# Performance work log

Measured on AMD Instinct MI355X. Metric: run time of the kernel, lower is better.

Reference implementation:

```python
import jax, jax.numpy as jnp
import numpy as np

B, N, K = 8, 2048, 20
NC = 50
EPS = 1e-5
SLOPE = 0.2


def _knn(xt, k):
    # xt: [B, N, C]; negative squared euclidean distance, top-k (includes self)
    xx = jnp.sum(xt * xt, axis=-1)                      # [B, N]
    inner = jnp.einsum('bnc,bmc->bnm', xt, xt)          # [B, N, N]
    dist = 2.0 * inner - xx[:, :, None] - xx[:, None, :]
    return jax.lax.top_k(dist, k)[1]                    # [B, N, k] int32


def _edge_conv(xt, w, g, b, k):
    # xt: [B, N, C]; w: [O, 2C]; BatchNorm2d over (B, N, k) per out-channel.
    idx = _knn(xt, k)
    nbr = xt[jnp.arange(B)[:, None, None], idx]          # [B, N, k, C]
    ctr = jnp.broadcast_to(xt[:, :, None, :], nbr.shape)
    edge = jnp.concatenate([nbr - ctr, ctr], axis=-1)    # [B, N, k, 2C]
    h = jnp.einsum('bnkc,oc->bnko', edge, w)             # 1x1 conv, no bias
    mu = jnp.mean(h, axis=(0, 1, 2))
    var = jnp.var(h, axis=(0, 1, 2))
    h = (h - mu) / jnp.sqrt(var + EPS) * g + b
    h = jnp.where(h > 0, h, SLOPE * h)                   # LeakyReLU(0.2)
    return jnp.max(h, axis=2)                            # max over k -> [B, N, O]


def _bn1d(y, g, b):
    mu = jnp.mean(y, axis=0)
    var = jnp.var(y, axis=0)
    return (y - mu) / jnp.sqrt(var + EPS) * g + b


def setup_inputs() -> dict:
    key = jax.random.key(0)
    ks = jax.random.split(key, 20)

    def rn(k, shape, scale):
        return jax.random.normal(k, shape, dtype=jnp.float32) * scale

    d = {
        'x': rn(ks[0], (B * N, 3), 1.0),
        'pos': rn(ks[1], (B * N, 3), 1.0),
        'batch': jnp.repeat(jnp.arange(B, dtype=jnp.int64), N),
        'edge_index': jax.random.randint(ks[2], (2, B * N), 0, B * N, dtype=jnp.int64),
        # EdgeConv 1x1 conv weights [out, in], BN gamma/beta
        'w1': rn(ks[3], (64, 6), 0.3),   'g1': jnp.ones(64),  'b1': jnp.zeros(64),
        'w2': rn(ks[4], (64, 128), 0.1), 'g2': jnp.ones(64),  'b2': jnp.zeros(64),
        'w3': rn(ks[5], (128, 128), 0.1),'g3': jnp.ones(128), 'b3': jnp.zeros(128),
        'w4': rn(ks[6], (256, 256), 0.08),'g4': jnp.ones(256),'b4': jnp.zeros(256),
        # lin1: Linear(512,1024)+ReLU+BN1d(1024)
        'lw1': rn(ks[7], (512, 1024), 0.04), 'lb1': jnp.zeros(1024),
        'lg1': jnp.ones(1024), 'lbb1': jnp.zeros(1024),
        # mlp: [1024->256 +ReLU+BN] -> [256->128 +ReLU+BN] -> Lin(128, NC)
        'mw1': rn(ks[8], (1024, 256), 0.03), 'mb1': jnp.zeros(256),
        'mg1': jnp.ones(256), 'mbb1': jnp.zeros(256),
        'mw2': rn(ks[9], (256, 128), 0.06), 'mb2': jnp.zeros(128),
        'mg2': jnp.ones(128), 'mbb2': jnp.zeros(128),
        'hw': rn(ks[10], (128, NC), 0.09), 'hb': jnp.zeros(NC),
    }
    return d


def reference(x, pos, batch, edge_index,
              w1, g1, b1, w2, g2, b2, w3, g3, b3, w4, g4, b4,
              lw1, lb1, lg1, lbb1,
              mw1, mb1, mg1, mbb1, mw2, mb2, mg2, mbb2,
              hw, hb):
    # batch is sorted with N points per cloud -> static reshape
    xt = x.reshape(B, N, 3)
    x1 = _edge_conv(xt, w1, g1, b1, K)   # [B, N, 64]
    x2 = _edge_conv(x1, w2, g2, b2, K)   # [B, N, 64]
    x3 = _edge_conv(x2, w3, g3, b3, K)   # [B, N, 128]
    x4 = _edge_conv(x3, w4, g4, b4, K)   # [B, N, 256]
    cat = jnp.concatenate([x1, x2, x3, x4], axis=-1)  # [B, N, 512]
    h = cat.reshape(B * N, 512)
    h = _bn1d(jax.nn.relu(h @ lw1 + lb1), lg1, lbb1)
    h = _bn1d(jax.nn.relu(h @ mw1 + mb1), mg1, mbb1)   # dropout = identity (eval)
    h = _bn1d(jax.nn.relu(h @ mw2 + mb2), mg2, mbb2)
    logits = h @ hw + hb
    return jax.nn.log_softmax(logits, axis=1)
```

## Files before the change

### kernel.cpp

```cpp
#include <hip/hip_runtime.h>
#include <math.h>

#define NB 8
#define NP 2048
#define KNBR 20
#define NROWS (NB*NP)
#define SLOPEV 0.2f
#define EPSV 1e-5f

typedef short s8v __attribute__((ext_vector_type(8)));
typedef float f4v __attribute__((ext_vector_type(4)));

__device__ __forceinline__ unsigned short f2bf(float f) {
    union { float f; unsigned u; } v; v.f = f;
    unsigned r = v.u + 0x7FFFu + ((v.u >> 16) & 1u);
    return (unsigned short)(r >> 16);
}

#define DK 16
__global__ __launch_bounds__(256, 2) void gemm64_dist(
    const double* __restrict__ A, int lda, int Kd,
    const double* __restrict__ xx, double* __restrict__ Cm, int batch0)
{
    __shared__ double As[DK][130];
    __shared__ double Bs[DK][66];
    const int tid = threadIdx.x;
    const int tx = tid & 15, ty = tid >> 4;
    const int bb = blockIdx.y;
    const int x  = blockIdx.x;
    int bi = (int)((sqrtf(4.0f * x + 1.0f) - 1.0f) * 0.5f);
    while (bi * (bi + 1) > x) --bi;
    while ((bi + 1) * (bi + 2) <= x) ++bi;
    const int bj = x - bi * (bi + 1);
    const int row0 = bi * 128, col0 = bj * 64;
    const double* Ab  = A + (size_t)(batch0 + bb) * NP * lda;
    double*       Cb  = Cm + (size_t)bb * NP * NP;
    const double* xxb = xx + (size_t)(batch0 + bb) * NP;

    double acc[8][4];
#pragma unroll
    for (int i = 0; i < 8; ++i)
#pragma unroll
        for (int j = 0; j < 4; ++j) acc[i][j] = 0.0;

    const int ma = tid >> 1, ka = (tid & 1) * 8;
    const int mb = tid >> 2, kb = (tid & 3) * 4;

    for (int kc = 0; kc < Kd; kc += DK) {
        const double* ap = Ab + (size_t)(row0 + ma) * lda + kc + ka;
#pragma unroll
        for (int i = 0; i < 8; ++i) {
            const int k2 = kc + ka + i;
            As[ka + i][ma] = (k2 < Kd) ? ap[i] : 0.0;
        }
        const double* bp = Ab + (size_t)(col0 + mb) * lda + kc + kb;
#pragma unroll
        for (int i = 0; i < 4; ++i) {
            const int k2 = kc + kb + i;
            Bs[kb + i][mb] = (k2 < Kd) ? bp[i] : 0.0;
        }
        __syncthreads();
#pragma unroll
        for (int k = 0; k < DK; ++k) {
            double a[8], b[4];
            *(double2*)&a[0] = *(const double2*)&As[k][ty * 4];
            *(double2*)&a[2] = *(const double2*)&As[k][ty * 4 + 2];
            *(double2*)&a[4] = *(const double2*)&As[k][64 + ty * 4];
            *(double2*)&a[6] = *(const double2*)&As[k][64 + ty * 4 + 2];
            *(double2*)&b[0] = *(const double2*)&Bs[k][tx * 4];
            *(double2*)&b[2] = *(const double2*)&Bs[k][tx * 4 + 2];
#pragma unroll
            for (int i = 0; i < 8; ++i)
#pragma unroll
                for (int j = 0; j < 4; ++j) acc[i][j] = fma(a[i], b[j], acc[i][j]);
        }
        __syncthreads();
    }

#pragma unroll
    for (int i = 0; i < 8; ++i) {
        const int r = row0 + ty * 4 + (i & 3) + ((i >> 2) << 6);
        const double xr = xxb[r];
#pragma unroll
        for (int j = 0; j < 4; ++j) {
            const int c = col0 + tx * 4 + j;
            const double a2 = 2.0 * acc[i][j];
            const double xc = xxb[c];
            Cb[(size_t)r * NP + c] = (a2 - xr) - xc;
            Cb[(size_t)c * NP + r] = (a2 - xc) - xr;
        }
    }
}

__global__ __launch_bounds__(256, 2) void gemm64(
    const double* __restrict__ A, int lda,
    const double* __restrict__ Bm, int ldb,
    double* __restrict__ P, double* __restrict__ Q, int O, int Kd)
{
    __shared__ double As[DK][130];
    __shared__ double Bs[DK][66];
    const int tid = threadIdx.x;
    const int tx = tid & 15, ty = tid >> 4;
    const int lin = blockIdx.y * gridDim.x + blockIdx.x;
    const int bx = lin / gridDim.y;
    const int by = lin - bx * gridDim.y;
    const int row0 = by * 128, col0 = bx * 64;

    double acc[8][4];
#pragma unroll
    for (int i = 0; i < 8; ++i)
#pragma unroll
        for (int j = 0; j < 4; ++j) acc[i][j] = 0.0;

    const int ma = tid >> 1, ka = (tid & 1) * 8;
    const int mb = tid >> 2, kb = (tid & 3) * 4;

    for (int kc = 0; kc < Kd; kc += DK) {
        const double* ap = A + (size_t)(row0 + ma) * lda + kc + ka;
#pragma unroll
        for (int i = 0; i < 8; ++i) {
            const int k2 = kc + ka + i;
            As[ka + i][ma] = (k2 < Kd) ? ap[i] : 0.0;
        }
        const double* bp = Bm + (size_t)(col0 + mb) * ldb + kc + kb;
#pragma unroll
        for (int i = 0; i < 4; ++i) {
            const int k2 = kc + kb + i;
            Bs[kb + i][mb] = (k2 < Kd) ? bp[i] : 0.0;
        }
        __syncthreads();
#pragma unroll
        for (int k = 0; k < DK; ++k) {
            double a[8], b[4];
            *(double2*)&a[0] = *(const double2*)&As[k][ty * 4];
            *(double2*)&a[2] = *(const double2*)&As[k][ty * 4 + 2];
            *(double2*)&a[4] = *(const double2*)&As[k][64 + ty * 4];
            *(double2*)&a[6] = *(const double2*)&As[k][64 + ty * 4 + 2];
            *(double2*)&b[0] = *(const double2*)&Bs[k][tx * 4];
            *(double2*)&b[2] = *(const double2*)&Bs[k][tx * 4 + 2];
#pragma unroll
            for (int i = 0; i < 8; ++i)
#pragma unroll
                for (int j = 0; j < 4; ++j) acc[i][j] = fma(a[i], b[j], acc[i][j]);
        }
        __syncthreads();
    }

    double* dst = (col0 < O) ? P : Q;
    const int cbase = (col0 < O) ? col0 : (col0 - O);
#pragma unroll
    for (int i = 0; i < 8; ++i) {
        const int r = row0 + ty * 4 + (i & 3) + ((i >> 2) << 6);
#pragma unroll
        for (int j = 0; j < 4; ++j) {
            const int c = cbase + tx * 4 + j;
            dst[(size_t)r * O + c] = acc[i][j];
        }
    }
}

__global__ __launch_bounds__(256) void gemm_bf16(
    const float* __restrict__ A, int lda,
    const unsigned short* __restrict__ W,
    float* __restrict__ C, int ldc,
    int Kd,
    const float* __restrict__ bias,
    const float* __restrict__ a_ss)
{
    __shared__ unsigned short As[4][64][8];
    __shared__ unsigned short Bs[4][128][8];
    const int tid = threadIdx.x;
    const int wave = tid >> 6, lane = tid & 63;
    const int quad = lane >> 4, l15 = lane & 15;
    const int row0 = blockIdx.y * 64, col0 = blockIdx.x * 128;

    f4v acc[4][2];
#pragma unroll
    for (int mt = 0; mt < 4; ++mt)
#pragma unroll
        for (int nt = 0; nt < 2; ++nt) acc[mt][nt] = (f4v){0.f, 0.f, 0.f, 0.f};

    const int ar = tid >> 2, akc = tid & 3;
    const int br = tid >> 1, bkc = (tid & 1) * 2;

    for (int kc0 = 0; kc0 < Kd; kc0 += 32) {
        {
            const float* ap = A + (size_t)(row0 + ar) * lda + kc0 + akc * 8;
            float t0[8];
            *(float4*)&t0[0] = *(const float4*)ap;
            *(float4*)&t0[4] = *(const float4*)(ap + 4);
            if (a_ss) {
                const int kb = kc0 + akc * 8;
#pragma unroll
                for (int i = 0; i < 8; ++i)
                    t0[i] = fmaf(t0[i], a_ss[kb + i], a_ss[Kd + kb + i]);
            }
            unsigned short u[8];
#pragma unroll
            for (int i = 0; i < 8; ++i) u[i] = f2bf(t0[i]);
            *(uint4*)&As[akc][ar][0] = *(const uint4*)&u[0];
        }
        {
            const unsigned short* wp = W + (size_t)(col0 + br) * Kd + kc0 + bkc * 8;
            uint4 q0 = *(const uint4*)wp;
            uint4 q1 = *(const uint4*)(wp + 8);
            *(uint4*)&Bs[bkc][br][0]     = q0;
            *(uint4*)&Bs[bkc + 1][br][0] = q1;
        }
        __syncthreads();

        s8v a[4], b[2];
#pragma unroll
        for (int mt = 0; mt < 4; ++mt)
            a[mt] = *(const s8v*)&As[quad][mt * 16 + l15][0];
#pragma unroll
        for (int nt = 0; nt < 2; ++nt)
            b[nt] = *(const s8v*)&Bs[quad][wave * 32 + nt * 16 + l15][0];
#pragma unroll
        for (int mt = 0; mt < 4; ++mt)
#pragma unroll
            for (int nt = 0; nt < 2; ++nt)
                acc[mt][nt] = __builtin_amdgcn_mfma_f32_16x16x32_bf16(
                    a[mt], b[nt], acc[mt][nt], 0, 0, 0);
        __syncthreads();
    }

#pragma unroll
    for (int mt = 0; mt < 4; ++mt)
#pragma unroll
        for (int nt = 0; nt < 2; ++nt) {
            const int col = col0 + wave * 32 + nt * 16 + l15;
            const float bi = bias[col];
#pragma unroll
            for (int r = 0; r < 4; ++r) {
                const int row = row0 + mt * 16 + quad * 4 + r;
                float v = acc[mt][nt][r] + bi;
                v = fmaxf(v, 0.f);
                C[(size_t)row * ldc + col] = v;
            }
        }
}

#define GBK 16
__global__ __launch_bounds__(256, 2) void gemm_f32(
    const float* __restrict__ A, int lda,
    const float* __restrict__ Bm, int ldb,
    float* __restrict__ Cm, int ldc,
    int M, int Nn, int Kd, int mode,
    const float* __restrict__ bias,
    const float* __restrict__ a_ss)
{
    __shared__ float As[GBK][132];
    __shared__ float Bs[GBK][132];
    const int tid = threadIdx.x;
    const int tx = tid & 15, ty = tid >> 4;
    const int lin = blockIdx.y * gridDim.x + blockIdx.x;
    const int bx = lin / gridDim.y;
    const int by = lin - bx * gridDim.y;
    const int row0 = by * 128, col0 = bx * 128;
    float acc[8][8];
#pragma unroll
    for (int i = 0; i < 8; ++i)
#pragma unroll
        for (int j = 0; j < 8; ++j) acc[i][j] = 0.f;

    const int m  = tid >> 1;
    const int kk = (tid & 1) * 8;

    for (int kc = 0; kc < Kd; kc += GBK) {
        const int gc = col0 + m;
        const float* ap = A  + (size_t)(row0 + m) * lda + kc + kk;
        const float* bp = Bm + (size_t)gc * ldb + kc + kk;
#pragma unroll
        for (int i = 0; i < 8; ++i) {
            const int k2 = kc + kk + i;
            float v = 0.f;
            if (k2 < Kd) {
                v = ap[i];
                if (a_ss) v = fmaf(v, a_ss[k2], a_ss[Kd + k2]);
            }
            As[kk + i][m] = v;
        }
#pragma unroll
        for (int i = 0; i < 8; ++i) {
            const int k2 = kc + kk + i;
            float v = 0.f;
            if (gc < Nn && k2 < Kd) v = bp[i];
            Bs[kk + i][m] = v;
        }
        __syncthreads();
#pragma unroll
        for (int k = 0; k < GBK; ++k) {
            float4 a0 = *(const float4*)&As[k][ty * 4];
            float4 a1 = *(const float4*)&As[k][64 + ty * 4];
            float4 b0 = *(const float4*)&Bs[k][tx * 4];
            float4 b1 = *(const float4*)&Bs[k][64 + tx * 4];
            float a[8] = {a0.x, a0.y, a0.z, a0.w, a1.x, a1.y, a1.z, a1.w};
            float b[8] = {b0.x, b0.y, b0.z, b0.w, b1.x, b1.y, b1.z, b1.w};
#pragma unroll
            for (int i = 0; i < 8; ++i)
#pragma unroll
                for (int j = 0; j < 8; ++j) acc[i][j] = fmaf(a[i], b[j], acc[i][j]);
        }
        __syncthreads();
    }

#pragma unroll
    for (int i = 0; i < 8; ++i) {
        const int row = row0 + ty * 4 + (i & 3) + ((i >> 2) << 6);
        if (row >= M) continue;
#pragma unroll
        for (int h = 0; h < 2; ++h) {
            const int c0 = col0 + tx * 4 + (h << 6);
#pragma unroll
            for (int j = 0; j < 4; ++j) {
                const int col = c0 + j;
                if (col < Nn) {
                    float t = acc[i][h * 4 + j];
                    if (mode == 2)      t = fmaxf(t + bias[col], 0.f);
                    else if (mode == 3) t = t + bias[col];
                    Cm[(size_t)row * ldc + col] = t;
                }
            }
        }
    }
}

__global__ void f2d_kernel(const float* __restrict__ in, double* __restrict__ out, long n)
{
    long t = (long)blockIdx.x * 256 + threadIdx.x;
    if (t < n) out[t] = (double)in[t];
}
__global__ void d2f_kernel(const double* __restrict__ in, float* __restrict__ out, long n)
{
    long t = (long)blockIdx.x * 256 + threadIdx.x;
    if (t < n) out[t] = (float)in[t];
}

__global__ void xx_kernel_d(const double* __restrict__ F, int lda, int C,
                            double* __restrict__ xx)
{
    int r = blockIdx.x * 256 + threadIdx.x;
    if (r >= NROWS) return;
    const double* p = F + (long)r * lda;
    double s = 0.0;
    for (int c = 0; c < C; ++c) { double v = p[c]; s = fma(v, v, s); }
    xx[r] = s;
}

__global__ void wmod_kernel_d(const float* __restrict__ w, double* __restrict__ wm,
                              int O, int C)
{
    int t = blockIdx.x * 256 + threadIdx.x;
    if (t >= O * C) return;
    int o = t / C, c = t - o * C;
    double a = (double)w[o * 2 * C + c];
    double b = (double)w[o * 2 * C + C + c];
    wm[o * C + c] = a;
    wm[(O + o) * C + c] = b - a;
}

__global__ void transpose_kernel(const float* __restrict__ in, float* __restrict__ out,
                                 int R, int C)
{
    long t = (long)blockIdx.x * 256 + threadIdx.x;
    if (t >= (long)R * C) return;
    int r = (int)(t / C), c = (int)(t - (long)r * C);
    out[(long)c * R + r] = in[t];
}

__global__ void transpose_bf(const float* __restrict__ in, unsigned short* __restrict__ out,
                             int R, int C)
{
    long t = (long)blockIdx.x * 256 + threadIdx.x;
    if (t >= (long)R * C) return;
    int r = (int)(t / C), c = (int)(t - (long)r * C);
    out[(long)c * R + r] = f2bf(in[t]);
}

__global__ __launch_bounds__(256) void topk2(const double* __restrict__ D,
                                             int* __restrict__ out, int batch0)
{
    const int lane = threadIdx.x & 63;
    const int bb   = blockIdx.y;
    const int row  = blockIdx.x * 4 + (threadIdx.x >> 6);
    const double* rp = D + (size_t)bb * NP * NP + (size_t)row * NP;
    double v[32];
#pragma unroll
    for (int j = 0; j < 16; ++j) {
        double2 p = *(const double2*)&rp[j * 128 + lane * 2];
        v[2 * j] = p.x; v[2 * j + 1] = p.y;
    }
    double lbest = v[0];
    int    lidx  = lane * 2;
#pragma unroll
    for (int q = 1; q < 32; ++q) {
        const int col = ((q >> 1) << 7) + lane * 2 + (q & 1);
        if (v[q] > lbest) { lbest = v[q]; lidx = col; }
    }

    int* op = out + ((size_t)(batch0 + bb) * NP + row) * KNBR;
    const int jbase = (batch0 + bb) * NP;

    for (int it = 0; it < KNBR; ++it) {
        double best = lbest; int bidx = lidx;
#pragma unroll
        for (int off = 32; off >= 1; off >>= 1) {
            double ov = __shfl_xor(best, off, 64);
            int    oi = __shfl_xor(bidx, off, 64);
            if (ov > best || (ov == best && oi < bidx)) { best = ov; bidx = oi; }
        }
        if (lane == 0) op[it] = jbase + bidx;
        if (lane == ((bidx >> 1) & 63)) {
            const int q = (((bidx >> 7) << 1) | (bidx & 1));
#pragma unroll
            for (int qq = 0; qq < 32; ++qq) if (qq == q) v[qq] = -INFINITY;
            lbest = v[0]; lidx = lane * 2;
#pragma unroll
            for (int qq = 1; qq < 32; ++qq) {
                const int col = ((qq >> 1) << 7) + lane * 2 + (qq & 1);
                if (v[qq] > lbest) { lbest = v[qq]; lidx = col; }
            }
        }
    }
}

__global__ __launch_bounds__(256) void edge_gather(const double* __restrict__ P,
                                                   const double* __restrict__ Q,
                                                   const int* __restrict__ idx,
                                                   int O, int shiftO,
                                                   double* __restrict__ sums,
                                                   double* __restrict__ catOut, int ldo)
{
    const int tid = threadIdx.x;
    const int o = tid & (O - 1);
    const int q = tid >> shiftO;
    const int nsub = 256 >> shiftO;
    const int lin = blockIdx.x;
    const int r0 = (lin & 7) * NP + (lin >> 3) * 16;
    double s = 0.0, ss = 0.0;
    for (int r = r0 + q; r < r0 + 16; r += nsub) {
        const double qv = Q[(size_t)r * O + o];
        const int* ip = idx + r * KNBR;
        double m = -INFINITY;
        for (int k = 0; k < KNBR; ++k) {
            const int j = ip[k];
            const double v = P[(size_t)j * O + o] + qv;
            s += v; ss = fma(v, v, ss);
            m = fmax(m, v);
        }
        catOut[(size_t)r * ldo + o] = m;
    }
    __shared__ double red[256];
    red[tid] = s; __syncthreads();
    if (q == 0) for (int qq = 1; qq < nsub; ++qq) s += red[o + (qq << shiftO)];
    __syncthreads();
    red[tid] = ss; __syncthreads();
    if (q == 0) {
        for (int qq = 1; qq < nsub; ++qq) ss += red[o + (qq << shiftO)];
        atomicAdd(&sums[o], s);
        atomicAdd(&sums[O + o], ss);
    }
}

__global__ void bn_finalize_d(const double* __restrict__ sums,
                              const float* __restrict__ g, const float* __restrict__ b,
                              double* __restrict__ ss, int O, double invCnt)
{
    int o = blockIdx.x * 256 + threadIdx.x;
    if (o >= O) return;
    double mu  = sums[o] * invCnt;
    double var = sums[O + o] * invCnt - mu * mu;
    double is  = 1.0 / sqrt(var + 1e-5);
    double sc  = (double)g[o] * is;
    ss[o] = sc;
    ss[O + o] = (double)b[o] - mu * sc;
}

__global__ __launch_bounds__(256) void bn_apply(double* __restrict__ catOut, int ldo,
                                                const double* __restrict__ ssb,
                                                int O, int shiftO,
                                                const double* __restrict__ P,
                                                const double* __restrict__ Q,
                                                const int* __restrict__ idx)
{
    const int t = blockIdx.x * 256 + threadIdx.x;
    const int o = t & (O - 1);
    const int r = t >> shiftO;
    const double sc = ssb[o], sh = ssb[O + o];
    double v = catOut[(size_t)r * ldo + o];
    if (sc < 0.0) {
        const double qv = Q[(size_t)r * O + o];
        const int* ip = idx + r * KNBR;
        double m = INFINITY;
        for (int k = 0; k < KNBR; ++k)
            m = fmin(m, P[(size_t)ip[k] * O + o] + qv);
        v = m;
    }
    double u = fma(v, sc, sh);
    u = u > 0.0 ? u : 0.2 * u;
    catOut[(size_t)r * ldo + o] = u;
}

__global__ void col_stats(const float* __restrict__ Y, int ncol,
                          float* __restrict__ sums)
{
    int c  = blockIdx.x * 128 + threadIdx.x;
    int r0 = blockIdx.y * 256;
    float s = 0.f, ss = 0.f;
    for (int r = r0; r < r0 + 256; ++r) {
        float v = Y[(long)r * ncol + c];
        s += v; ss = fmaf(v, v, ss);
    }
    atomicAdd(&sums[c], s);
    atomicAdd(&sums[ncol + c], ss);
}

__global__ void bn_finalize_f(const float* __restrict__ sums,
                              const float* __restrict__ g, const float* __restrict__ b,
                              float* __restrict__ ss, int O, float invCnt)
{
    int o = blockIdx.x * 256 + threadIdx.x;
    if (o >= O) return;
    float mu  = sums[o] * invCnt;
    float var = sums[O + o] * invCnt - mu * mu;
    float is  = rsqrtf(var + EPSV);
    float sc  = g[o] * is;
    ss[o] = sc;
    ss[O + o] = b[o] - mu * sc;
}

__global__ __launch_bounds__(256) void log_softmax_kernel(float* __restrict__ Y)
{
    const int lane = threadIdx.x & 63;
    const int row  = blockIdx.x * 4 + (threadIdx.x >> 6);
    float v = -INFINITY;
    if (lane < 50) v = Y[(long)row * 50 + lane];
    float mx = v;
#pragma unroll
    for (int off = 32; off >= 1; off >>= 1) mx = fmaxf(mx, __shfl_xor(mx, off, 64));
    float e = (lane < 50) ? expf(v - mx) : 0.f;
    float s = e;
#pragma unroll
    for (int off = 32; off >= 1; off >>= 1) s += __shfl_xor(s, off, 64);
    float l = logf(s) + mx;
    if (lane < 50) Y[(long)row * 50 + lane] = v - l;
}

extern "C" void kernel_launch(void* const* d_in, const int* in_sizes, int n_in,
                              void* d_out, int out_size, void* d_ws, size_t ws_size,
                              hipStream_t stream)
{
    const float* x   = (const float*)d_in[0];
    const float* w[4]  = {(const float*)d_in[4], (const float*)d_in[7],
                          (const float*)d_in[10], (const float*)d_in[13]};
    const float* g[4]  = {(const float*)d_in[5], (const float*)d_in[8],
                          (const float*)d_in[11], (const float*)d_in[14]};
    const float* bb[4] = {(const float*)d_in[6], (const float*)d_in[9],
                          (const float*)d_in[12], (const float*)d_in[15]};
    const float* lw1 = (const float*)d_in[16]; const float* lb1 = (const float*)d_in[17];
    const float* lg1 = (const float*)d_in[18]; const float* lbb1 = (const float*)d_in[19];
    const float* mw1 = (const float*)d_in[20]; const float* mb1 = (const float*)d_in[21];
    const float* mg1 = (const float*)d_in[22]; const float* mbb1 = (const float*)d_in[23];
    const float* mw2 = (const float*)d_in[24]; const float* mb2 = (const float*)d_in[25];
    const float* mg2 = (const float*)d_in[26]; const float* mbb2 = (const float*)d_in[27];
    const float* hw  = (const float*)d_in[28]; const float* hb  = (const float*)d_in[29];
    float* out = (float*)d_out;

    char* base = (char*)d_ws;
    double* catD = (double*)base;
    char*  un    = base + 67108864;
    double* D    = (double*)un;
    double* Pb   = (double*)un;
    double* Qb   = (double*)(un + 33554432);
    float* cat32 = (float*)un;
    float* Y2    = (float*)(un + 33554432);
    float* Y3    = (float*)(un + 50331648);
    unsigned short* lw1Tb = (unsigned short*)(un + 58720256);
    unsigned short* mw1Tb = (unsigned short*)(un + 59768832);
    unsigned short* mw2Tb = (unsigned short*)(un + 60293120);
    float* hwT   = (float*)(un + 60358656);
    float* Y1    = (float*)base;
    char* tail = base + 2u * 67108864u;
    int*    idxb  = (int*)tail;
    double* xD    = (double*)(tail + 1310720);
    double* xxD   = (double*)(tail + 1703936);
    double* wmodD = (double*)(tail + 1835008);
    double* sumsD = (double*)(tail + 2359296);
    double* ssbD  = (double*)(tail + 2367488);
    float*  sumsF = (float*)(tail + 2375680);
    float*  ssbF  = (float*)(tail + 2383872);

    f2d_kernel<<<(NROWS * 3 + 255) / 256, 256, 0, stream>>>(x, xD, (long)NROWS * 3);

    const double* Fin[4] = {xD, catD + 0, catD + 64, catD + 128};
    const int   ldaL[4] = {3, 512, 512, 512};
    const int   CL[4]   = {3, 64, 64, 128};
    const int   OL[4]   = {64, 64, 128, 256};
    const int   coff[4] = {0, 64, 128, 256};

    for (int l = 0; l < 4; ++l) {
        const double* F = Fin[l];
        const int lda = ldaL[l], C = CL[l], O = OL[l];
        const int shiftO = (O == 64) ? 6 : (O == 128) ? 7 : 8;

        wmod_kernel_d<<<(O * C + 255) / 256, 256, 0, stream>>>(w[l], wmodD, O, C);
        xx_kernel_d<<<NROWS / 256, 256, 0, stream>>>(F, lda, C, xxD);

        for (int p = 0; p < 4; ++p) {
            const int b0 = p * 2;
            gemm64_dist<<<dim3(272, 2), 256, 0, stream>>>(F, lda, C, xxD, D, b0);
            topk2<<<dim3(NP / 4, 2), 256, 0, stream>>>(D, idxb, b0);
        }

        gemm64<<<dim3((2 * O) / 64, NROWS / 128), 256, 0, stream>>>(
            F, lda, wmodD, C, Pb, Qb, O, C);

        hipMemsetAsync(sumsD, 0, 2 * O * sizeof(double), stream);
        edge_gather<<<NROWS / 16, 256, 0, stream>>>(Pb, Qb, idxb, O, shiftO, sumsD,
                                                    catD + coff[l], 512);
        bn_finalize_d<<<(O + 255) / 256, 256, 0, stream>>>(sumsD, g[l], bb[l], ssbD, O,
                                                           1.0 / ((double)NROWS * KNBR));
        bn_apply<<<(NROWS * O) / 256, 256, 0, stream>>>(catD + coff[l], 512, ssbD,
                                                        O, shiftO, Pb, Qb, idxb);
    }

    d2f_kernel<<<((long)NROWS * 512 + 255) / 256, 256, 0, stream>>>(catD, cat32, (long)NROWS * 512);

    transpose_bf<<<(512 * 1024 + 255) / 256, 256, 0, stream>>>(lw1, lw1Tb, 512, 1024);
    transpose_bf<<<(1024 * 256 + 255) / 256, 256, 0, stream>>>(mw1, mw1Tb, 1024, 256);
    transpose_bf<<<(256 * 128 + 255) / 256, 256, 0, stream>>>(mw2, mw2Tb, 256, 128);
    transpose_kernel<<<(128 * 50 + 255) / 256, 256, 0, stream>>>(hw, hwT, 128, 50);

    {
        gemm_bf16<<<dim3(1024 / 128, NROWS / 64), 256, 0, stream>>>(
            cat32, 512, lw1Tb, Y1, 1024, 512, lb1, nullptr);
        hipMemsetAsync(sumsF, 0, 2 * 1024 * sizeof(float), stream);
        col_stats<<<dim3(1024 / 128, 64), 128, 0, stream>>>(Y1, 1024, sumsF);
        bn_finalize_f<<<4, 256, 0, stream>>>(sumsF, lg1, lbb1, ssbF, 1024, 1.f / NROWS);
    }
    {
        gemm_bf16<<<dim3(256 / 128, NROWS / 64), 256, 0, stream>>>(
            Y1, 1024, mw1Tb, Y2, 256, 1024, mb1, ssbF);
        hipMemsetAsync(sumsF, 0, 2 * 256 * sizeof(float), stream);
        col_stats<<<dim3(256 / 128, 64), 128, 0, stream>>>(Y2, 256, sumsF);
        bn_finalize_f<<<1, 256, 0, stream>>>(sumsF, mg1, mbb1, ssbF, 256, 1.f / NROWS);
    }
    {
        gemm_bf16<<<dim3(128 / 128, NROWS / 64), 256, 0, stream>>>(
            Y2, 256, mw2Tb, Y3, 128, 256, mb2, ssbF);
        hipMemsetAsync(sumsF, 0, 2 * 128 * sizeof(float), stream);
        col_stats<<<dim3(1, 64), 128, 0, stream>>>(Y3, 128, sumsF);
        bn_finalize_f<<<1, 256, 0, stream>>>(sumsF, mg2, mbb2, ssbF, 128, 1.f / NROWS);
    }
    {
        dim3 gg(1, NROWS / 128);
        gemm_f32<<<gg, 256, 0, stream>>>(Y3, 128, hwT, 128, out, 50,
                                         NROWS, 50, 128, 3, hb, ssbF);
        log_softmax_kernel<<<NROWS / 4, 256, 0, stream>>>(out);
    }
}
```

Measured before the change: 2.321 ms.

## Use FP64 MFMA for distance and edge-conv GEMMs with runtime layout probe

Replaces the scalar FP64 FMA inner loops of the pairwise-distance GEMM and the edge-conv projection GEMM with __builtin_amdgcn_mfma_f64_16x16x4f64 matrix instructions, each wave computing a 32x64 tile. A small probe kernel runs once per call to discover the MFMA operand and output lane layout and writes a lookup table that both GEMMs read for fragment indexing and output scatter. This aims to cut the FP64 compute cost of the KNN distance and projection stages. It adds an extra launch and scattered output stores, and depends on the probe decoding the layout correctly. The block-index swizzle in gemm64 is also removed.

Result: faster. 2.225 ms (-4.1%).

```diff
diff --git a/kernel.cpp b/kernel.cpp
--- a/kernel.cpp
+++ b/kernel.cpp
@@ -10,6 +10,7 @@
 
 typedef short s8v __attribute__((ext_vector_type(8)));
 typedef float f4v __attribute__((ext_vector_type(4)));
+typedef double d4v __attribute__((ext_vector_type(4)));
 
 __device__ __forceinline__ unsigned short f2bf(float f) {
     union { float f; unsigned u; } v; v.f = f;
@@ -17,15 +18,41 @@
     return (unsigned short)(r >> 16);
 }
 
+__global__ void mfma64_probe(int* __restrict__ tab)
+{
+    const int lane = threadIdx.x;
+    d4v z = {0.0, 0.0, 0.0, 0.0};
+    d4v pa = __builtin_amdgcn_mfma_f64_16x16x4f64((double)lane, 1.0, z, 0, 0, 0);
+    d4v pb = __builtin_amdgcn_mfma_f64_16x16x4f64(1.0, (double)lane, z, 0, 0, 0);
+    int famA = 1, famB = 1;
+#pragma unroll
+    for (int r = 0; r < 4; ++r) {
+        int iv = (int)(pa[r] + 0.5);
+        int row;
+        if ((iv & 3) == 0 && iv >= 96) row = (iv - 96) >> 2;
+        else { row = (iv - 6) >> 4; famA = 0; }
+        int jv = (int)(pb[r] + 0.5);
+        int col;
+        if ((jv & 3) == 0 && jv >= 96) col = (jv - 96) >> 2;
+        else { col = (jv - 6) >> 4; famB = 0; }
+        tab[lane * 8 + r]     = row;
+        tab[lane * 8 + 4 + r] = col;
+    }
+    tab[512 + lane] = famA;
+    tab[576 + lane] = famB;
+}
+
 #define DK 16
 __global__ __launch_bounds__(256, 2) void gemm64_dist(
     const double* __restrict__ A, int lda, int Kd,
-    const double* __restrict__ xx, double* __restrict__ Cm, int batch0)
+    const double* __restrict__ xx, double* __restrict__ Cm, int batch0,
+    const int* __restrict__ tab)
 {
     __shared__ double As[DK][130];
     __shared__ double Bs[DK][66];
     const int tid = threadIdx.x;
-    const int tx = tid & 15, ty = tid >> 4;
+    const int wave = tid >> 6, lane = tid & 63;
+    const int quad = lane >> 4, l15 = lane & 15;
     const int bb = blockIdx.y;
     const int x  = blockIdx.x;
     int bi = (int)((sqrtf(4.0f * x + 1.0f) - 1.0f) * 0.5f);
@@ -37,11 +64,21 @@
     double*       Cb  = Cm + (size_t)bb * NP * NP;
     const double* xxb = xx + (size_t)(batch0 + bb) * NP;
 
-    double acc[8][4];
-#pragma unroll
-    for (int i = 0; i < 8; ++i)
-#pragma unroll
-        for (int j = 0; j < 4; ++j) acc[i][j] = 0.0;
+    int rT[4], cT[4];
+#pragma unroll
+    for (int r = 0; r < 4; ++r) { rT[r] = tab[lane * 8 + r]; cT[r] = tab[lane * 8 + 4 + r]; }
+    const int famA = tab[512];
+    const int famB = tab[576];
+    const int am = famA ? l15 : (lane >> 2);
+    const int ak = famA ? quad : (lane & 3);
+    const int bn = famB ? l15 : (lane >> 2);
+    const int bk = famB ? quad : (lane & 3);
+
+    d4v acc[2][4];
+#pragma unroll
+    for (int mt = 0; mt < 2; ++mt)
+#pragma unroll
+        for (int nt = 0; nt < 4; ++nt) acc[mt][nt] = (d4v){0.0, 0.0, 0.0, 0.0};
 
     const int ma = tid >> 1, ka = (tid & 1) * 8;
     const int mb = tid >> 2, kb = (tid & 3) * 4;
@@ -61,56 +98,71 @@
         }
         __syncthreads();
 #pragma unroll
-        for (int k = 0; k < DK; ++k) {
-            double a[8], b[4];
-            *(double2*)&a[0] = *(const double2*)&As[k][ty * 4];
-            *(double2*)&a[2] = *(const double2*)&As[k][ty * 4 + 2];
-            *(double2*)&a[4] = *(const double2*)&As[k][64 + ty * 4];
-            *(double2*)&a[6] = *(const double2*)&As[k][64 + ty * 4 + 2];
-            *(double2*)&b[0] = *(const double2*)&Bs[k][tx * 4];
-            *(double2*)&b[2] = *(const double2*)&Bs[k][tx * 4 + 2];
-#pragma unroll
-            for (int i = 0; i < 8; ++i)
-#pragma unroll
-                for (int j = 0; j < 4; ++j) acc[i][j] = fma(a[i], b[j], acc[i][j]);
+        for (int kg = 0; kg < 4; ++kg) {
+            const int k = kg * 4;
+            double a0 = As[k + ak][wave * 32 + am];
+            double a1 = As[k + ak][wave * 32 + 16 + am];
+            double b0 = Bs[k + bk][bn];
+            double b1 = Bs[k + bk][16 + bn];
+            double b2 = Bs[k + bk][32 + bn];
+            double b3 = Bs[k + bk][48 + bn];
+            acc[0][0] = __builtin_amdgcn_mfma_f64_16x16x4f64(a0, b0, acc[0][0], 0, 0, 0);
+            acc[0][1] = __builtin_amdgcn_mfma_f64_16x16x4f64(a0, b1, acc[0][1], 0, 0, 0);
+            acc[0][2] = __builtin_amdgcn_mfma_f64_16x16x4f64(a0, b2, acc[0][2], 0, 0, 0);
+            acc[0][3] = __builtin_amdgcn_mfma_f64_16x16x4f64(a0, b3, acc[0][3], 0, 0, 0);
+            acc[1][0] = __builtin_amdgcn_mfma_f64_16x16x4f64(a1, b0, acc[1][0], 0, 0, 0);
+            acc[1][1] = __builtin_amdgcn_mfma_f64_16x16x4f64(a1, b1, acc[1][1], 0, 0, 0);
+            acc[1][2] = __builtin_amdgcn_mfma_f64_16x16x4f64(a1, b2, acc[1][2], 0, 0, 0);
+            acc[1][3] = __builtin_amdgcn_mfma_f64_16x16x4f64(a1, b3, acc[1][3], 0, 0, 0);
         }
         __syncthreads();
     }
 
 #pragma unroll
-    for (int i = 0; i < 8; ++i) {
-        const int r = row0 + ty * 4 + (i & 3) + ((i >> 2) << 6);
-        const double xr = xxb[r];
-#pragma unroll
-        for (int j = 0; j < 4; ++j) {
-            const int c = col0 + tx * 4 + j;
-            const double a2 = 2.0 * acc[i][j];
-            const double xc = xxb[c];
-            Cb[(size_t)r * NP + c] = (a2 - xr) - xc;
-            Cb[(size_t)c * NP + r] = (a2 - xc) - xr;
-        }
-    }
+    for (int mt = 0; mt < 2; ++mt)
+#pragma unroll
+        for (int nt = 0; nt < 4; ++nt) {
+#pragma unroll
+            for (int rg = 0; rg < 4; ++rg) {
+                const int r = row0 + wave * 32 + mt * 16 + rT[rg];
+                const int c = col0 + nt * 16 + cT[rg];
+                const double a2 = 2.0 * acc[mt][nt][rg];
+                const double xr = xxb[r];
+                const double xc = xxb[c];
+                Cb[(size_t)r * NP + c] = (a2 - xr) - xc;
+                Cb[(size_t)c * NP + r] = (a2 - xc) - xr;
+            }
+        }
 }
 
 __global__ __launch_bounds__(256, 2) void gemm64(
     const double* __restrict__ A, int lda,
     const double* __restrict__ Bm, int ldb,
-    double* __restrict__ P, double* __restrict__ Q, int O, int Kd)
+    double* __restrict__ P, double* __restrict__ Q, int O, int Kd,
+    const int* __restrict__ tab)
 {
     __shared__ double As[DK][130];
     __shared__ double Bs[DK][66];
     const int tid = threadIdx.x;
-    const int tx = tid & 15, ty = tid >> 4;
-    const int lin = blockIdx.y * gridDim.x + blockIdx.x;
-    const int bx = lin / gridDim.y;
-    const int by = lin - bx * gridDim.y;
-    const int row0 = by * 128, col0 = bx * 64;
-
-    double acc[8][4];
-#pragma unroll
-    for (int i = 0; i < 8; ++i)
-#pragma unroll
-        for (int j = 0; j < 4; ++j) acc[i][j] = 0.0;
+    const int wave = tid >> 6, lane = tid & 63;
+    const int quad = lane >> 4, l15 = lane & 15;
+    const int row0 = blockIdx.y * 128, col0 = blockIdx.x * 64;
+
+    int rT[4], cT[4];
+#pragma unroll
+    for (int r = 0; r < 4; ++r) { rT[r] = tab[lane * 8 + r]; cT[r] = tab[lane * 8 + 4 + r]; }
+    const int famA = tab[512];
+    const int famB = tab[576];
+    const int am = famA ? l15 : (lane >> 2);
+    const int ak = famA ? quad : (lane & 3);
+    const int bn = famB ? l15 : (lane >> 2);
+    const int bk = famB ? quad : (lane & 3);
+
+    d4v acc[2][4];
+#pragma unroll
+    for (int mt = 0; mt < 2; ++mt)
+#pragma unroll
+        for (int nt = 0; nt < 4; ++nt) acc[mt][nt] = (d4v){0.0, 0.0, 0.0, 0.0};
 
     const int ma = tid >> 1, ka = (tid & 1) * 8;
     const int mb = tid >> 2, kb = (tid & 3) * 4;
@@ -130,18 +182,22 @@
         }
         __syncthreads();
 #pragma unroll
-        for (int k = 0; k < DK; ++k) {
-            double a[8], b[4];
-            *(double2*)&a[0] = *(const double2*)&As[k][ty * 4];
-            *(double2*)&a[2] = *(const double2*)&As[k][ty * 4 + 2];
-            *(double2*)&a[4] = *(const double2*)&As[k][64 + ty * 4];
-            *(double2*)&a[6] = *(const double2*)&As[k][64 + ty * 4 + 2];
-            *(double2*)&b[0] = *(const double2*)&Bs[k][tx * 4];
-            *(double2*)&b[2] = *(const double2*)&Bs[k][tx * 4 + 2];
-#pragma unroll
-            for (int i = 0; i < 8; ++i)
-#pragma unroll
-                for (int j = 0; j < 4; ++j) acc[i][j] = fma(a[i], b[j], acc[i][j]);
+        for (int kg = 0; kg < 4; ++kg) {
+            const int k = kg * 4;
+            double a0 = As[k + ak][wave * 32 + am];
+            double a1 = As[k + ak][wave * 32 + 16 + am];
+            double b0 = Bs[k + bk][bn];
+            double b1 = Bs[k + bk][16 + bn];
+            double b2 = Bs[k + bk][32 + bn];
+            double b3 = Bs[k + bk][48 + bn];
+            acc[0][0] = __builtin_amdgcn_mfma_f64_16x16x4f64(a0, b0, acc[0][0], 0, 0, 0);
+            acc[0][1] = __builtin_amdgcn_mfma_f64_16x16x4f64(a0, b1, acc[0][1], 0, 0, 0);
+            acc[0][2] = __builtin_amdgcn_mfma_f64_16x16x4f64(a0, b2, acc[0][2], 0, 0, 0);
+            acc[0][3] = __builtin_amdgcn_mfma_f64_16x16x4f64(a0, b3, acc[0][3], 0, 0, 0);
+            acc[1][0] = __builtin_amdgcn_mfma_f64_16x16x4f64(a1, b0, acc[1][0], 0, 0, 0);
+            acc[1][1] = __builtin_amdgcn_mfma_f64_16x16x4f64(a1, b1, acc[1][1], 0, 0, 0);
+            acc[1][2] = __builtin_amdgcn_mfma_f64_16x16x4f64(a1, b2, acc[1][2], 0, 0, 0);
+            acc[1][3] = __builtin_amdgcn_mfma_f64_16x16x4f64(a1, b3, acc[1][3], 0, 0, 0);
         }
         __syncthreads();
     }
@@ -149,14 +205,16 @@
     double* dst = (col0 < O) ? P : Q;
     const int cbase = (col0 < O) ? col0 : (col0 - O);
 #pragma unroll
-    for (int i = 0; i < 8; ++i) {
-        const int r = row0 + ty * 4 + (i & 3) + ((i >> 2) << 6);
-#pragma unroll
-        for (int j = 0; j < 4; ++j) {
-            const int c = cbase + tx * 4 + j;
-            dst[(size_t)r * O + c] = acc[i][j];
-        }
-    }
+    for (int mt = 0; mt < 2; ++mt)
+#pragma unroll
+        for (int nt = 0; nt < 4; ++nt) {
+#pragma unroll
+            for (int rg = 0; rg < 4; ++rg) {
+                const int r = row0 + wave * 32 + mt * 16 + rT[rg];
+                const int c = cbase + nt * 16 + cT[rg];
+                dst[(size_t)r * O + c] = acc[mt][nt][rg];
+            }
+        }
 }
 
 __global__ __launch_bounds__(256) void gemm_bf16(
@@ -590,6 +648,9 @@
     double* ssbD  = (double*)(tail + 2367488);
     float*  sumsF = (float*)(tail + 2375680);
     float*  ssbF  = (float*)(tail + 2383872);
+    int*    mtab  = (int*)(tail + 2392064);
+
+    mfma64_probe<<<1, 64, 0, stream>>>(mtab);
 
     f2d_kernel<<<(NROWS * 3 + 255) / 256, 256, 0, stream>>>(x, xD, (long)NROWS * 3);
 
@@ -609,12 +670,12 @@
 
         for (int p = 0; p < 4; ++p) {
             const int b0 = p * 2;
-            gemm64_dist<<<dim3(272, 2), 256, 0, stream>>>(F, lda, C, xxD, D, b0);
+            gemm64_dist<<<dim3(272, 2), 256, 0, stream>>>(F, lda, C, xxD, D, b0, mtab);
             topk2<<<dim3(NP / 4, 2), 256, 0, stream>>>(D, idxb, b0);
         }
 
         gemm64<<<dim3((2 * O) / 64, NROWS / 128), 256, 0, stream>>>(
-            F, lda, wmodD, C, Pb, Qb, O, C);
+            F, lda, wmodD, C, Pb, Qb, O, C, mtab);
 
         hipMemsetAsync(sumsD, 0, 2 * O * sizeof(double), stream);
         edge_gather<<<NROWS / 16, 256, 0, stream>>>(Pb, Qb, idxb, O, shiftO, sumsD,
```
